# Performance work log

Measured on AMD Instinct MI355X. Metric: run time of the kernel, lower is better.

Reference implementation:

```python
import jax, jax.numpy as jnp
import numpy as np

B, S, NX, H = 8, 1024, 1024, 16
D = NX // H  # head_features = 64
SCALE = True


def setup_inputs() -> dict:
    key = jax.random.key(0)
    k1, k2, k3 = jax.random.split(key, 3)
    x = jax.random.normal(k1, (B, S, NX), dtype=jnp.float32)
    w_attn = jax.random.normal(k2, (NX, 3 * NX), dtype=jnp.float32) * 0.02
    b_attn = jnp.zeros((3 * NX,), dtype=jnp.float32)
    w_proj = jax.random.normal(k3, (NX, NX), dtype=jnp.float32) * 0.02
    b_proj = jnp.zeros((NX,), dtype=jnp.float32)
    return {"x": x, "w_attn": w_attn, "b_attn": b_attn, "w_proj": w_proj, "b_proj": b_proj}


def _split_heads(t):
    # (B, S, NX) -> (B, H, S, D)
    return t.reshape(B, S, H, D).transpose(0, 2, 1, 3)


def reference(x, w_attn, b_attn, w_proj, b_proj):
    # fused QKV projection (Conv1D): addmm over flattened tokens
    qkv = x @ w_attn + b_attn                      # (B, S, 3*NX)
    q, k, v = jnp.split(qkv, 3, axis=-1)
    q = _split_heads(q)                            # (B, H, S, D)
    k = _split_heads(k)
    v = _split_heads(v)

    w = jnp.einsum("bhqd,bhkd->bhqk", q, k)        # full S x S scores
    if SCALE:
        w = w / jnp.sqrt(jnp.asarray(D, w.dtype))
    # causal mask applied exactly as in the source: multiply + big-negative subtract
    b = jnp.tril(jnp.ones((S, S), dtype=w.dtype))[None, None]
    w = w * b - 1e10 * (1.0 - b)
    w = jax.nn.softmax(w, axis=-1)                 # attn_pdrop = 0 (eval)
    a = jnp.einsum("bhqk,bhkd->bhqd", w, v)        # (B, H, S, D)

    # merge heads: (B, H, S, D) -> (B, S, NX)
    a = a.transpose(0, 2, 1, 3).reshape(B, S, NX)
    a = a @ w_proj + b_proj                        # c_proj; resid_pdrop = 0 (eval)
    return a
```

## Files before the change

### kernel.cpp

```cpp
#include <hip/hip_runtime.h>
#include <hip/hip_bf16.h>

#define BB 8
#define SS 1024
#define NXX 1024
#define HH 16
#define DD 64
#define MM (BB * SS)

typedef __attribute__((ext_vector_type(8))) short short8;
typedef __attribute__((ext_vector_type(4))) short short4v;
typedef __attribute__((ext_vector_type(4))) float float4v;

static __device__ inline short bf16bits(float v) {
    __hip_bfloat16 t = __float2bfloat16(v);
    return *reinterpret_cast<short*>(&t);
}

__global__ __launch_bounds__(256) void prep_kernel(
    const float* __restrict__ x, __hip_bfloat16* __restrict__ xb,
    const float* __restrict__ w_attn, __hip_bfloat16* __restrict__ wT_attn,
    const float* __restrict__ w_proj, __hip_bfloat16* __restrict__ wT_proj)
{
    __shared__ __hip_bfloat16 tile[32][33];
    const int blk = blockIdx.x;
    const int tid = threadIdx.x;

    if (blk < 8192) {
        int i = blk * 1024 + tid * 4;
        float4 v = *(const float4*)(x + i);
        xb[i + 0] = __float2bfloat16(v.x);
        xb[i + 1] = __float2bfloat16(v.y);
        xb[i + 2] = __float2bfloat16(v.z);
        xb[i + 3] = __float2bfloat16(v.w);
        return;
    }
    const float* W;
    __hip_bfloat16* Wt;
    int K, N, idx;
    if (blk < 8192 + 3072) { idx = blk - 8192;  W = w_attn; Wt = wT_attn; K = NXX; N = 3 * NXX; }
    else                   { idx = blk - 11264; W = w_proj; Wt = wT_proj; K = NXX; N = NXX; }
    const int k0 = (idx % (K / 32)) * 32;
    const int n0 = (idx / (K / 32)) * 32;
    const int tx = tid % 32;
    const int ty = tid / 32;
#pragma unroll
    for (int p = 0; p < 4; ++p) {
        int k = ty + p * 8;
        tile[k][tx] = __float2bfloat16(W[(size_t)(k0 + k) * N + n0 + tx]);
    }
    __syncthreads();
#pragma unroll
    for (int p = 0; p < 4; ++p) {
        int nn = ty + p * 8;
        Wt[(size_t)(n0 + nn) * K + k0 + tx] = tile[tx][nn];
    }
}

#define STAGE2(SRC, DST, kk)                                                   \
    {                                                                          \
        _Pragma("unroll") for (int j_ = 0; j_ < 2; ++j_) {                     \
            const __hip_bfloat16* s_ = (SRC) + (size_t)(j_ * 128) * K + (kk);  \
            char* d_ = (char*)(DST) + j_ * 8192 + (wave << 10);                \
            __builtin_amdgcn_global_load_lds(                                  \
                (const __attribute__((address_space(1))) void*)s_,             \
                (__attribute__((address_space(3))) void*)d_, 16, 0, 0);        \
        }                                                                      \
    }

#define WAIT_LGKM0_FENCED()                                                    \
    asm volatile("s_waitcnt lgkmcnt(0)" ::: "memory");                         \
    __builtin_amdgcn_sched_barrier(0);

template <int MODE>
__global__ __launch_bounds__(512, 2) void gemm256(
    const __hip_bfloat16* __restrict__ A,
    const __hip_bfloat16* __restrict__ Bt,
    const float* __restrict__ bias,
    void* __restrict__ Cv,
    __hip_bfloat16* __restrict__ vT,
    int M, int K, int N)
{
    __shared__ __attribute__((aligned(16))) char smem[65536];

    const int tid  = threadIdx.x;
    const int wave = tid >> 6;
    const int lane = tid & 63;
    const int wr = wave >> 2;
    const int wc = wave & 3;

    const int nwg = (int)gridDim.x;
    const int cpx = nwg >> 3;
    const int bid = (int)blockIdx.x;
    const int swz = (bid & 7) * cpx + (bid >> 3);
    const int mtiles = M >> 8;
    const int m0 = (swz % mtiles) << 8;
    const int n0 = (swz / mtiles) << 8;

    const int NT = K >> 5;

    const int row_s  = tid >> 2;
    const int srccol = (((tid & 3) ^ ((tid >> 3) & 3)) << 3);
    const __hip_bfloat16* aSrc = A  + (size_t)(m0 + row_s) * K + srccol;
    const __hip_bfloat16* bSrc = Bt + (size_t)(n0 + row_s) * K + srccol;

    const int l15 = lane & 15, q4 = lane >> 4;
    const int skey = (l15 >> 1) & 3;
    const int sslot = (q4 ^ skey) << 4;
    const int offA = ((wr << 7) + l15) * 64 + sslot;
    const int offB = 16384 + ((wc << 6) + l15) * 64 + sslot;

    float4v acc[8][4];
#pragma unroll
    for (int i = 0; i < 8; ++i)
#pragma unroll
        for (int j = 0; j < 4; ++j) acc[i][j] = (float4v){0.f, 0.f, 0.f, 0.f};

    STAGE2(aSrc, smem, 0);
    STAGE2(bSrc, smem + 16384, 0);
    if (NT > 1) {
        STAGE2(bSrc, smem + 32768 + 16384, 32);
        asm volatile("s_waitcnt vmcnt(2)" ::: "memory");
    } else {
        asm volatile("s_waitcnt vmcnt(0)" ::: "memory");
    }
    __builtin_amdgcn_s_barrier();

    for (int t = 0; t < NT; ++t) {
        char* bufc = (char*)smem + ((t & 1) << 15);
        char* bufn = (char*)smem + (((t + 1) & 1) << 15);
        const char* Ab = bufc;

        short8 a[8], b[4];

#pragma unroll
        for (int mf = 0; mf < 4; ++mf) a[mf] = *(const short8*)(Ab + offA + mf * 1024);
#pragma unroll
        for (int nf = 0; nf < 4; ++nf) b[nf] = *(const short8*)(bufc + offB + nf * 1024);
        if (t + 1 < NT) STAGE2(aSrc, bufn, (t + 1) << 5);
        __builtin_amdgcn_s_barrier();
        WAIT_LGKM0_FENCED();
        __builtin_amdgcn_s_setprio(1);
#pragma unroll
        for (int mf = 0; mf < 4; ++mf)
#pragma unroll
            for (int nf = 0; nf < 4; ++nf)
                acc[mf][nf] = __builtin_amdgcn_mfma_f32_16x16x32_bf16(
                    a[mf], b[nf], acc[mf][nf], 0, 0, 0);
        __builtin_amdgcn_s_setprio(0);
        __builtin_amdgcn_s_barrier();

#pragma unroll
        for (int mf = 0; mf < 4; ++mf) a[mf + 4] = *(const short8*)(Ab + offA + (mf + 4) * 1024);
        if (t + 2 < NT) {
            STAGE2(bSrc, bufc + 16384, (t + 2) << 5);
            asm volatile("s_waitcnt vmcnt(2)" ::: "memory");
        } else if (t + 1 < NT) {
            asm volatile("s_waitcnt vmcnt(0)" ::: "memory");
        }
        __builtin_amdgcn_s_barrier();
        WAIT_LGKM0_FENCED();
        __builtin_amdgcn_s_setprio(1);
#pragma unroll
        for (int mf = 0; mf < 4; ++mf)
#pragma unroll
            for (int nf = 0; nf < 4; ++nf)
                acc[mf + 4][nf] = __builtin_amdgcn_mfma_f32_16x16x32_bf16(
                    a[mf + 4], b[nf], acc[mf + 4][nf], 0, 0, 0);
        __builtin_amdgcn_s_setprio(0);
        __builtin_amdgcn_s_barrier();
    }

    const int cr = q4 * 4;
    const int cc = l15;

    if (MODE == 1 && n0 >= 2048) {
        const int bb = m0 / SS;
#pragma unroll
        for (int mf = 0; mf < 8; ++mf) {
            int grow = m0 + (wr << 7) + mf * 16 + cr;
            int ssr = grow & (SS - 1);
#pragma unroll
            for (int nf = 0; nf < 4; ++nf) {
                int gcol = n0 + (wc << 6) + nf * 16 + cc;
                float bv = bias[gcol];
                int col = gcol - 2048;
                int hh = col >> 6, dd = col & 63;
                short4v pk;
#pragma unroll
                for (int r = 0; r < 4; ++r) pk[r] = bf16bits(acc[mf][nf][r] + bv);
                *(short4v*)(vT + (size_t)((bb * HH + hh) * 64 + dd) * SS + ssr) = pk;
            }
        }
    } else {
        const float qs = (MODE == 1 && n0 < 1024) ? 0.125f : 1.0f;
#pragma unroll
        for (int mf = 0; mf < 8; ++mf) {
            int grow = m0 + (wr << 7) + mf * 16 + cr;
#pragma unroll
            for (int nf = 0; nf < 4; ++nf) {
                int gcol = n0 + (wc << 6) + nf * 16 + cc;
                float bv = bias[gcol];
#pragma unroll
                for (int r = 0; r < 4; ++r) {
                    float v = (acc[mf][nf][r] + bv) * qs;
                    if constexpr (MODE == 1)
                        ((__hip_bfloat16*)Cv)[(size_t)(grow + r) * N + gcol] =
                            __float2bfloat16(v);
                    else
                        ((float*)Cv)[(size_t)(grow + r) * N + gcol] = v;
                }
            }
        }
    }
}

#define PSTR 72

__global__ __launch_bounds__(256) void attn_mfma_kernel(
    const __hip_bfloat16* __restrict__ qkv,
    const __hip_bfloat16* __restrict__ vT,
    __hip_bfloat16* __restrict__ aout)
{
    const int bh = blockIdx.x;
    const int b = bh / HH, h = bh % HH;
    const int q0 = ((int)gridDim.y - 1 - (int)blockIdx.y) * 128;

    __shared__ __hip_bfloat16 Ks[64 * PSTR];
    __shared__ __hip_bfloat16 Vs[64 * PSTR];
    __shared__ __hip_bfloat16 Ps[4][32 * PSTR];

    const int tid  = threadIdx.x;
    const int wave = tid >> 6;
    const int lane = tid & 63;
    const int quad = lane >> 4;
    const int l16  = lane & 15;

    short8 qf[2][2];
#pragma unroll
    for (int t = 0; t < 2; ++t) {
        const __hip_bfloat16* qp = qkv +
            (size_t)(b * SS + q0 + wave * 32 + t * 16 + l16) * 3072 + h * 64 + quad * 8;
        qf[t][0] = *(const short8*)qp;
        qf[t][1] = *(const short8*)(qp + 32);
    }

    float4v o_acc[2][4];
    float l_acc[2][4];
#pragma unroll
    for (int t = 0; t < 2; ++t)
#pragma unroll
        for (int nt = 0; nt < 4; ++nt) o_acc[t][nt] = (float4v){0.f, 0.f, 0.f, 0.f};
#pragma unroll
    for (int t = 0; t < 2; ++t)
#pragma unroll
        for (int r = 0; r < 4; ++r) l_acc[t][r] = 0.f;

    const int sk  = tid & 63;
    const int sdo = (tid >> 6) * 16;
    const int vd  = tid >> 2;
    const int vko = (tid & 3) * 16;
    const int qmin_w = q0 + wave * 32;
    const int nkt = q0 / 64 + 2;

    for (int kt = 0; kt < nkt; ++kt) {
        const int k0 = kt * 64;
        __syncthreads();
        {
            const __hip_bfloat16* kr =
                qkv + (size_t)(b * SS + k0 + sk) * 3072 + 1024 + h * 64 + sdo;
            *(short8*)&Ks[sk * PSTR + sdo]     = *(const short8*)kr;
            *(short8*)&Ks[sk * PSTR + sdo + 8] = *(const short8*)(kr + 8);
            const __hip_bfloat16* vr = vT + (size_t)(bh * 64 + vd) * SS + k0 + vko;
            *(short8*)&Vs[vd * PSTR + vko]     = *(const short8*)vr;
            *(short8*)&Vs[vd * PSTR + vko + 8] = *(const short8*)(vr + 8);
        }
        __syncthreads();
        if (k0 > qmin_w + 31) continue;

        const short* ks = (const short*)Ks;
        float4v sacc[2][4];
#pragma unroll
        for (int t = 0; t < 2; ++t)
#pragma unroll
            for (int nt = 0; nt < 4; ++nt) sacc[t][nt] = (float4v){0.f, 0.f, 0.f, 0.f};
#pragma unroll
        for (int kc = 0; kc < 2; ++kc)
#pragma unroll
            for (int nt = 0; nt < 4; ++nt) {
                short8 kb = *(const short8*)(ks + (nt * 16 + l16) * PSTR + kc * 32 + quad * 8);
                sacc[0][nt] = __builtin_amdgcn_mfma_f32_16x16x32_bf16(qf[0][kc], kb, sacc[0][nt], 0, 0, 0);
                sacc[1][nt] = __builtin_amdgcn_mfma_f32_16x16x32_bf16(qf[1][kc], kb, sacc[1][nt], 0, 0, 0);
            }

        const bool needmask = (k0 + 63 > qmin_w);
        __hip_bfloat16* pw = Ps[wave];
#pragma unroll
        for (int t = 0; t < 2; ++t)
#pragma unroll
            for (int nt = 0; nt < 4; ++nt) {
                int kk = k0 + nt * 16 + l16;
#pragma unroll
                for (int r = 0; r < 4; ++r) {
                    float s = sacc[t][nt][r];
                    if (needmask) {
                        int qq = qmin_w + t * 16 + quad * 4 + r;
                        if (kk > qq) s = -1e10f;
                    }
                    float p = __expf(s);
                    l_acc[t][r] += p;
                    pw[(t * 16 + quad * 4 + r) * PSTR + nt * 16 + l16] =
                        __float2bfloat16(p);
                }
            }

        const short* ps = (const short*)pw;
        const short* vs = (const short*)Vs;
#pragma unroll
        for (int kc = 0; kc < 2; ++kc) {
            short8 pa0 = *(const short8*)(ps + (0 * 16 + l16) * PSTR + kc * 32 + quad * 8);
            short8 pa1 = *(const short8*)(ps + (1 * 16 + l16) * PSTR + kc * 32 + quad * 8);
#pragma unroll
            for (int nt = 0; nt < 4; ++nt) {
                short8 vb = *(const short8*)(vs + (nt * 16 + l16) * PSTR + kc * 32 + quad * 8);
                o_acc[0][nt] = __builtin_amdgcn_mfma_f32_16x16x32_bf16(pa0, vb, o_acc[0][nt], 0, 0, 0);
                o_acc[1][nt] = __builtin_amdgcn_mfma_f32_16x16x32_bf16(pa1, vb, o_acc[1][nt], 0, 0, 0);
            }
        }
    }

#pragma unroll
    for (int t = 0; t < 2; ++t)
#pragma unroll
        for (int r = 0; r < 4; ++r) {
            float l = l_acc[t][r];
            l += __shfl_xor(l, 1);
            l += __shfl_xor(l, 2);
            l += __shfl_xor(l, 4);
            l += __shfl_xor(l, 8);
            float inv = 1.f / l;
            int row = q0 + wave * 32 + t * 16 + quad * 4 + r;
            __hip_bfloat16* op = aout + (size_t)(b * SS + row) * NXX + h * 64 + l16;
#pragma unroll
            for (int nt = 0; nt < 4; ++nt)
                op[nt * 16] = __float2bfloat16(o_acc[t][nt][r] * inv);
        }
}

extern "C" void kernel_launch(void* const* d_in, const int* in_sizes, int n_in,
                              void* d_out, int out_size, void* d_ws, size_t ws_size,
                              hipStream_t stream)
{
    const float* x      = (const float*)d_in[0];
    const float* w_attn = (const float*)d_in[1];
    const float* b_attn = (const float*)d_in[2];
    const float* w_proj = (const float*)d_in[3];
    const float* b_proj = (const float*)d_in[4];
    float* out = (float*)d_out;

    char* ws = (char*)d_ws;
    __hip_bfloat16* qkv     = (__hip_bfloat16*)ws;
    __hip_bfloat16* vT      = (__hip_bfloat16*)(ws + (size_t)48 * 1024 * 1024);
    __hip_bfloat16* xb      = (__hip_bfloat16*)(ws + (size_t)64 * 1024 * 1024);
    __hip_bfloat16* amid    = xb;
    __hip_bfloat16* wT_attn = (__hip_bfloat16*)(ws + (size_t)80 * 1024 * 1024);
    __hip_bfloat16* wT_proj = (__hip_bfloat16*)(ws + (size_t)86 * 1024 * 1024);

    prep_kernel<<<dim3(12288), dim3(256), 0, stream>>>(
        x, xb, w_attn, wT_attn, w_proj, wT_proj);

    gemm256<1><<<dim3((MM / 256) * ((3 * NXX) / 256)), dim3(512), 0, stream>>>(
        xb, wT_attn, b_attn, qkv, vT, MM, NXX, 3 * NXX);

    attn_mfma_kernel<<<dim3(BB * HH, SS / 128), dim3(256), 0, stream>>>(qkv, vT, amid);

    gemm256<0><<<dim3((MM / 256) * (NXX / 256)), dim3(512), 0, stream>>>(
        amid, wT_proj, b_proj, out, nullptr, MM, NXX, NXX);
}
```

Baseline: 245.5 us.

## Switch GEMM to 256x128 tiles with triple-buffered A and grouped tile swizzle

The GEMM kernels move from 256x256 output tiles to 256x128 tiles. This doubles the grid and halves the accumulator registers per wave, with waves now laid out 4x2 over 64x64 sub-tiles. A is staged through three LDS buffers and B through two, so loads run two K-steps ahead. Workgroups are remapped in groups of 8 M-tiles to improve L2 reuse. The cost is lower arithmetic intensity per tile, since each A tile is loaded twice as often.

```diff
diff --git a/kernel.cpp b/kernel.cpp
--- a/kernel.cpp
+++ b/kernel.cpp
@@ -57,15 +57,24 @@
     }
 }
 
-#define STAGE2(SRC, DST, kk)                                                   \
+#define STAGE_A(DST, kk)                                                       \
     {                                                                          \
         _Pragma("unroll") for (int j_ = 0; j_ < 2; ++j_) {                     \
-            const __hip_bfloat16* s_ = (SRC) + (size_t)(j_ * 128) * K + (kk);  \
+            const __hip_bfloat16* s_ = aSrc + (size_t)(j_ * 128) * K + (kk);   \
             char* d_ = (char*)(DST) + j_ * 8192 + (wave << 10);                \
             __builtin_amdgcn_global_load_lds(                                  \
                 (const __attribute__((address_space(1))) void*)s_,             \
                 (__attribute__((address_space(3))) void*)d_, 16, 0, 0);        \
         }                                                                      \
+    }
+
+#define STAGE_B(DST, kk)                                                       \
+    {                                                                          \
+        const __hip_bfloat16* s_ = bSrc + (kk);                                \
+        char* d_ = (char*)(DST) + (wave << 10);                                \
+        __builtin_amdgcn_global_load_lds(                                      \
+            (const __attribute__((address_space(1))) void*)s_,                 \
+            (__attribute__((address_space(3))) void*)d_, 16, 0, 0);            \
     }
 
 #define WAIT_LGKM0_FENCED()                                                    \
@@ -86,16 +95,19 @@
     const int tid  = threadIdx.x;
     const int wave = tid >> 6;
     const int lane = tid & 63;
-    const int wr = wave >> 2;
-    const int wc = wave & 3;
+    const int wm = (wave >> 1) << 6;
+    const int wn = (wave & 1) << 6;
 
     const int nwg = (int)gridDim.x;
     const int cpx = nwg >> 3;
     const int bid = (int)blockIdx.x;
     const int swz = (bid & 7) * cpx + (bid >> 3);
-    const int mtiles = M >> 8;
-    const int m0 = (swz % mtiles) << 8;
-    const int n0 = (swz / mtiles) << 8;
+    const int ntN = N >> 7;
+    const int width = ntN << 3;
+    const int group = swz / width;
+    const int w = swz % width;
+    const int m0 = ((group << 3) + (w & 7)) << 8;
+    const int n0 = (w >> 3) << 7;
 
     const int NT = K >> 5;
 
@@ -105,44 +117,44 @@
     const __hip_bfloat16* bSrc = Bt + (size_t)(n0 + row_s) * K + srccol;
 
     const int l15 = lane & 15, q4 = lane >> 4;
-    const int skey = (l15 >> 1) & 3;
-    const int sslot = (q4 ^ skey) << 4;
-    const int offA = ((wr << 7) + l15) * 64 + sslot;
-    const int offB = 16384 + ((wc << 6) + l15) * 64 + sslot;
-
-    float4v acc[8][4];
-#pragma unroll
-    for (int i = 0; i < 8; ++i)
+    const int sslot = (q4 ^ ((l15 >> 1) & 3)) << 4;
+    const int offA = (wm + l15) * 64 + sslot;
+    const int offB = (wn + l15) * 64 + sslot;
+
+    float4v acc[4][4];
+#pragma unroll
+    for (int i = 0; i < 4; ++i)
 #pragma unroll
         for (int j = 0; j < 4; ++j) acc[i][j] = (float4v){0.f, 0.f, 0.f, 0.f};
 
-    STAGE2(aSrc, smem, 0);
-    STAGE2(bSrc, smem + 16384, 0);
-    if (NT > 1) {
-        STAGE2(bSrc, smem + 32768 + 16384, 32);
-        asm volatile("s_waitcnt vmcnt(2)" ::: "memory");
-    } else {
-        asm volatile("s_waitcnt vmcnt(0)" ::: "memory");
-    }
+    char* const Abuf0 = (char*)smem;
+    char* const Bbuf0 = (char*)smem + 49152;
+
+    STAGE_A(Abuf0,          0);
+    STAGE_B(Bbuf0,          0);
+    STAGE_A(Abuf0 + 16384, 32);
+    STAGE_B(Bbuf0 +  8192, 32);
+    asm volatile("s_waitcnt vmcnt(3)" ::: "memory");
     __builtin_amdgcn_s_barrier();
 
+    int ia = 0;
     for (int t = 0; t < NT; ++t) {
-        char* bufc = (char*)smem + ((t & 1) << 15);
-        char* bufn = (char*)smem + (((t + 1) & 1) << 15);
-        const char* Ab = bufc;
-
-        short8 a[8], b[4];
-
-#pragma unroll
-        for (int mf = 0; mf < 4; ++mf) a[mf] = *(const short8*)(Ab + offA + mf * 1024);
-#pragma unroll
-        for (int nf = 0; nf < 4; ++nf) b[nf] = *(const short8*)(bufc + offB + nf * 1024);
-        if (t + 1 < NT) STAGE2(aSrc, bufn, (t + 1) << 5);
+        const char* Ab = Abuf0 + ia * 16384;
+        char* Bb = Bbuf0 + ((t & 1) << 13);
+        const int ia2 = (ia == 0) ? 2 : ia - 1;
+
+        short8 a[4], b[4];
+
+#pragma unroll
+        for (int mf = 0; mf < 2; ++mf) a[mf] = *(const short8*)(Ab + offA + mf * 1024);
+#pragma unroll
+        for (int nf = 0; nf < 4; ++nf) b[nf] = *(const short8*)(Bb + offB + nf * 1024);
+        if (t + 2 < NT) STAGE_A(Abuf0 + ia2 * 16384, (t + 2) << 5);
         __builtin_amdgcn_s_barrier();
         WAIT_LGKM0_FENCED();
         __builtin_amdgcn_s_setprio(1);
 #pragma unroll
-        for (int mf = 0; mf < 4; ++mf)
+        for (int mf = 0; mf < 2; ++mf)
 #pragma unroll
             for (int nf = 0; nf < 4; ++nf)
                 acc[mf][nf] = __builtin_amdgcn_mfma_f32_16x16x32_bf16(
@@ -151,10 +163,10 @@
         __builtin_amdgcn_s_barrier();
 
 #pragma unroll
-        for (int mf = 0; mf < 4; ++mf) a[mf + 4] = *(const short8*)(Ab + offA + (mf + 4) * 1024);
+        for (int mf = 2; mf < 4; ++mf) a[mf] = *(const short8*)(Ab + offA + mf * 1024);
         if (t + 2 < NT) {
-            STAGE2(bSrc, bufc + 16384, (t + 2) << 5);
-            asm volatile("s_waitcnt vmcnt(2)" ::: "memory");
+            STAGE_B(Bb, (t + 2) << 5);
+            asm volatile("s_waitcnt vmcnt(3)" ::: "memory");
         } else if (t + 1 < NT) {
             asm volatile("s_waitcnt vmcnt(0)" ::: "memory");
         }
@@ -162,13 +174,15 @@
         WAIT_LGKM0_FENCED();
         __builtin_amdgcn_s_setprio(1);
 #pragma unroll
-        for (int mf = 0; mf < 4; ++mf)
+        for (int mf = 2; mf < 4; ++mf)
 #pragma unroll
             for (int nf = 0; nf < 4; ++nf)
-                acc[mf + 4][nf] = __builtin_amdgcn_mfma_f32_16x16x32_bf16(
-                    a[mf + 4], b[nf], acc[mf + 4][nf], 0, 0, 0);
+                acc[mf][nf] = __builtin_amdgcn_mfma_f32_16x16x32_bf16(
+                    a[mf], b[nf], acc[mf][nf], 0, 0, 0);
         __builtin_amdgcn_s_setprio(0);
         __builtin_amdgcn_s_barrier();
+
+        ia = (ia == 2) ? 0 : ia + 1;
     }
 
     const int cr = q4 * 4;
@@ -177,12 +191,12 @@
     if (MODE == 1 && n0 >= 2048) {
         const int bb = m0 / SS;
 #pragma unroll
-        for (int mf = 0; mf < 8; ++mf) {
-            int grow = m0 + (wr << 7) + mf * 16 + cr;
+        for (int mf = 0; mf < 4; ++mf) {
+            int grow = m0 + wm + mf * 16 + cr;
             int ssr = grow & (SS - 1);
 #pragma unroll
             for (int nf = 0; nf < 4; ++nf) {
-                int gcol = n0 + (wc << 6) + nf * 16 + cc;
+                int gcol = n0 + wn + nf * 16 + cc;
                 float bv = bias[gcol];
                 int col = gcol - 2048;
                 int hh = col >> 6, dd = col & 63;
@@ -195,11 +209,11 @@
     } else {
         const float qs = (MODE == 1 && n0 < 1024) ? 0.125f : 1.0f;
 #pragma unroll
-        for (int mf = 0; mf < 8; ++mf) {
-            int grow = m0 + (wr << 7) + mf * 16 + cr;
+        for (int mf = 0; mf < 4; ++mf) {
+            int grow = m0 + wm + mf * 16 + cr;
 #pragma unroll
             for (int nf = 0; nf < 4; ++nf) {
-                int gcol = n0 + (wc << 6) + nf * 16 + cc;
+                int gcol = n0 + wn + nf * 16 + cc;
                 float bv = bias[gcol];
 #pragma unroll
                 for (int r = 0; r < 4; ++r) {
@@ -369,11 +383,11 @@
     prep_kernel<<<dim3(12288), dim3(256), 0, stream>>>(
         x, xb, w_attn, wT_attn, w_proj, wT_proj);
 
-    gemm256<1><<<dim3((MM / 256) * ((3 * NXX) / 256)), dim3(512), 0, stream>>>(
+    gemm256<1><<<dim3((MM / 256) * ((3 * NXX) / 128)), dim3(512), 0, stream>>>(
         xb, wT_attn, b_attn, qkv, vT, MM, NXX, 3 * NXX);
 
     attn_mfma_kernel<<<dim3(BB * HH, SS / 128), dim3(256), 0, stream>>>(qkv, vT, amid);
 
-    gemm256<0><<<dim3((MM / 256) * (NXX / 256)), dim3(512), 0, stream>>>(
+    gemm256<0><<<dim3((MM / 256) * (NXX / 128)), dim3(512), 0, stream>>>(
         amid, wT_proj, b_proj, out, nullptr, MM, NXX, NXX);
 }
```

After: 215.5 us. 1.14x faster.
